# Kernel tuning notes

Measured on AMD Instinct MI355X. Metric: run time of the kernel, lower is better.

The kernel has to match this reference:

```python
import jax, jax.numpy as jnp
import numpy as np

N, E = 3200, 50000
RBF, HID = 16, 128
CUT = 5.0
NS, NV = 32, 16            # multiplicities of 0e and 1o blocks
D = NS + 3 * NV            # 80 = node/message irrep dim
WNUM = NS*NS + NV*NS + NS*NV + NV*NV  # 2304 tensor-product weights per edge
EPS = 1e-8
# path normalization (fully-connected TP, 2 paths per output irrep)
A1 = 1.0 / np.sqrt(2.0 * NS)
A2 = 1.0 / np.sqrt(2.0 * NV)
A3 = 1.0 / np.sqrt(2.0 * NS)
A4 = 1.0 / np.sqrt(2.0 * NV)
ISQ3 = 1.0 / np.sqrt(3.0)


def setup_inputs() -> dict:
    key = jax.random.key(0)
    ks = jax.random.split(key, 24)
    nrm = lambda k, s, sc=1.0: jax.random.normal(k, s, jnp.float32) * sc
    x = nrm(ks[0], (N, D))
    edge_src = jax.random.randint(ks[1], (E,), 0, N)
    edge_dst = jax.random.randint(ks[2], (E,), 0, N)
    dirs = nrm(ks[3], (E, 3))
    unit = dirs / jnp.linalg.norm(dirs, axis=1, keepdims=True)
    # component-normalized SH for l=0,1: [1, sqrt(3)*r_hat]
    edge_sh = jnp.concatenate([jnp.ones((E, 1), jnp.float32), np.sqrt(3.0) * unit], axis=1)
    edge_rbf = nrm(ks[4], (E, RBF))
    edge_len = jax.random.uniform(ks[5], (E,), jnp.float32, 0.1, 6.0)  # some beyond cutoff
    inp = dict(x=x, edge_src=edge_src, edge_dst=edge_dst, edge_sh=edge_sh,
               edge_rbf=edge_rbf, edge_len=edge_len)
    # IrrepNorm affine params
    inp['norm_w'] = jnp.ones((D,), jnp.float32)
    inp['norm_b'] = jnp.zeros((D,), jnp.float32)
    # radial weight MLP (RBF -> HID -> HID -> WNUM)
    inp['mw1'] = nrm(ks[6], (RBF, HID), 1.0/np.sqrt(RBF)); inp['mb1'] = jnp.zeros((HID,), jnp.float32)
    inp['mw2'] = nrm(ks[7], (HID, HID), 1.0/np.sqrt(HID)); inp['mb2'] = jnp.zeros((HID,), jnp.float32)
    inp['mw3'] = nrm(ks[8], (HID, WNUM), 1.0/np.sqrt(HID)); inp['mb3'] = jnp.zeros((WNUM,), jnp.float32)
    # edge gate MLP (RBF -> HID -> 1)
    inp['gw1'] = nrm(ks[9], (RBF, HID), 1.0/np.sqrt(RBF)); inp['gb1'] = jnp.zeros((HID,), jnp.float32)
    inp['gw2'] = nrm(ks[10], (HID, 1), 1.0/np.sqrt(HID)); inp['gb2'] = jnp.zeros((1,), jnp.float32)
    # equivariant linears (e3nn stores N(0,1) weights, normalizes by 1/sqrt(fan_in))
    inp['Ws'] = nrm(ks[11], (NS, NS + NV))   # msg_linear scalar part: 32 -> 32 scalars + 16 gates
    inp['Wv'] = nrm(ks[12], (NV, NV))        # msg_linear vector part
    inp['Us'] = nrm(ks[13], (NS, NS))        # update_linear
    inp['Uv'] = nrm(ks[14], (NV, NV))
    inp['Ss'] = nrm(ks[15], (NS, NS))        # self_linear
    inp['Sv'] = nrm(ks[16], (NV, NV))
    inp['res_scale'] = jnp.float32(0.1)
    return inp


def _irrep_norm(x, w, b):
    s = x[:, :NS]
    v = x[:, NS:].reshape(-1, NV, 3)
    mean = s.mean(axis=1, keepdims=True)
    var = ((s - mean) ** 2).mean(axis=1, keepdims=True)
    s = (s - mean) / jnp.sqrt(var + EPS)
    rms = jnp.sqrt((v ** 2).mean(axis=2, keepdims=True) + EPS)
    v = v / rms
    out = jnp.concatenate([s, v.reshape(-1, 3 * NV)], axis=-1)
    return out * w + b


def reference(x, edge_src, edge_dst, edge_sh, edge_rbf, edge_len,
              norm_w, norm_b, mw1, mb1, mw2, mb2, mw3, mb3,
              gw1, gb1, gw2, gb2, Ws, Wv, Us, Uv, Ss, Sv, res_scale):
    silu = jax.nn.silu
    x_norm = _irrep_norm(x, norm_w, norm_b)                  # [N, 80]
    # radial tensor-product weights per edge
    h = silu(edge_rbf @ mw1 + mb1)
    h = silu(h @ mw2 + mb2)
    tpw = h @ mw3 + mb3                                      # [E, 2304]
    o1 = NS*NS; o2 = o1 + NV*NS; o3 = o2 + NS*NV
    w1 = tpw[:, :o1].reshape(-1, NS, NS)
    w2 = tpw[:, o1:o2].reshape(-1, NV, NS)
    w3 = tpw[:, o2:o3].reshape(-1, NS, NV)
    w4 = tpw[:, o3:].reshape(-1, NV, NV)
    # gather source node features
    xs = x_norm[edge_src, :NS]                               # [E, 32]
    xv = x_norm[edge_src, NS:].reshape(-1, NV, 3)            # [E, 16, 3]
    sh0 = edge_sh[:, 0]                                      # [E]
    sh1 = edge_sh[:, 1:4]                                    # [E, 3]
    # fully-connected TP paths
    msg_s = A1 * jnp.einsum('ei,eio->eo', xs * sh0[:, None], w1)
    inner = jnp.einsum('eim,em->ei', xv, sh1) * ISQ3         # 1o x 1o -> 0e
    msg_s = msg_s + A2 * jnp.einsum('ei,eio->eo', inner, w2)
    msg_v = A3 * jnp.einsum('ei,eio->eo', xs, w3)[:, :, None] * sh1[:, None, :]
    msg_v = msg_v + A4 * jnp.einsum('eim,eio->eom', xv, w4) * sh0[:, None, None]
    m = jnp.concatenate([msg_s, msg_v.reshape(-1, 3 * NV)], axis=-1)  # [E, 80]
    # cutoff envelope and learned edge gate
    cutoff_w = 0.5 * (jnp.cos(jnp.pi * edge_len / CUT) + 1.0) * (edge_len <= CUT).astype(x.dtype)
    gate_w = jax.nn.sigmoid(silu(edge_rbf @ gw1 + gb1) @ gw2 + gb2)   # [E, 1]
    edge_w = cutoff_w[:, None] * gate_w                               # [E, 1]
    m = m * edge_w
    # scatter-add aggregate + normalization
    agg = jax.ops.segment_sum(m, edge_dst, num_segments=N)            # [N, 80]
    den = jax.ops.segment_sum(edge_w, edge_dst, num_segments=N)       # [N, 1]
    agg = agg / jnp.maximum(den, 1e-8)
    # msg_linear -> scalars + gates + gated vectors
    ag_s = agg[:, :NS]
    ag_v = agg[:, NS:].reshape(-1, NV, 3)
    sc = (ag_s @ Ws) / np.sqrt(NS)                                    # [N, 48]
    vc = jnp.einsum('nim,io->nom', ag_v, Wv) / np.sqrt(NV)            # [N, 16, 3]
    s_g = silu(sc[:, :NS])
    gates = jax.nn.sigmoid(sc[:, NS:])
    v_g = vc * gates[:, :, None]
    # update + self interaction
    upd_s = (s_g @ Us) / np.sqrt(NS)
    upd_v = jnp.einsum('nim,io->nom', v_g, Uv) / np.sqrt(NV)
    self_s = (x_norm[:, :NS] @ Ss) / np.sqrt(NS)
    self_v = jnp.einsum('nim,io->nom', x_norm[:, NS:].reshape(-1, NV, 3), Sv) / np.sqrt(NV)
    out = jnp.concatenate([self_s + upd_s, (self_v + upd_v).reshape(-1, 3 * NV)], axis=-1)
    return x + res_scale * out
```

## Files before the change

kernel.cpp:

```cpp
#include <hip/hip_runtime.h>
#include <hip/hip_bf16.h>
#include <math.h>

#define N_NODES 3200
#define E_EDGES 50000
#define RBFN 16
#define HID 128
#define NS 32
#define NV 16
#define DD 80
#define WNUM 2304
#define CUTF 5.0f
#define EPSF 1e-8f

#define A1C 0.125f
#define A2C 0.17677669529663687f
#define A3C 0.125f
#define A4C 0.17677669529663687f
#define A2ISQ 0.10206207261596575f

typedef __attribute__((ext_vector_type(4))) float f32x4;
typedef __attribute__((ext_vector_type(8))) short bf16x8;

__device__ __forceinline__ float sigm(float x) { return 1.0f / (1.0f + __expf(-x)); }
__device__ __forceinline__ float silu_f(float x) { return x * sigm(x); }

__device__ __forceinline__ short bf16r(float x) {
    union { float f; unsigned u; } v; v.f = x;
    unsigned r = (v.u + 0x7fffu + ((v.u >> 16) & 1u)) >> 16;
    return (short)r;
}
__device__ __forceinline__ float b2f(unsigned short s) {
    union { float f; unsigned u; } v; v.u = ((unsigned)s) << 16; return v.f;
}

__global__ void k_scan(const int* __restrict__ hist, int* __restrict__ start) {
    __shared__ int part[256];
    int t = threadIdx.x;
    int loc[13];
    int s = 0;
#pragma unroll
    for (int j = 0; j < 13; j++) {
        int idx = t * 13 + j;
        int v = (idx < N_NODES) ? hist[idx] : 0;
        loc[j] = s; s += v;
    }
    part[t] = s;
    __syncthreads();
    for (int off = 1; off < 256; off <<= 1) {
        int v = part[t];
        int add = (t >= off) ? part[t - off] : 0;
        __syncthreads();
        part[t] = v + add;
        __syncthreads();
    }
    int pre = (t == 0) ? 0 : part[t - 1];
#pragma unroll
    for (int j = 0; j < 13; j++) {
        int idx = t * 13 + j;
        if (idx < N_NODES) start[idx] = pre + loc[j];
    }
    if (t == 255) start[N_NODES] = part[255];
}

__global__ void k_scatter(const int* __restrict__ edst, const int* __restrict__ start,
                          int* __restrict__ cur, int* __restrict__ perm) {
    int e = blockIdx.x * 256 + threadIdx.x;
    if (e < E_EDGES) {
        int d = edst[e];
        int pos = start[d] + atomicAdd(&cur[d], 1);
        perm[pos] = e;
    }
}

__global__ void k_prep0(const float* __restrict__ mw2, __hip_bfloat16* __restrict__ mw2f) {
    __shared__ __hip_bfloat16 st[2048];
    int t = blockIdx.x, tid = threadIdx.x;
    for (int idx = tid; idx < 2048; idx += 256) {
        int k = idx >> 4, c = idx & 15;
        float v = mw2[k * HID + t * 16 + c];
        int kk = k >> 5, q4 = (k >> 3) & 3, j = k & 7;
        st[kk * 512 + (q4 * 16 + c) * 8 + j] = __float2bfloat16(v);
    }
    __syncthreads();
    ((bf16x8*)(mw2f + t * 2048))[tid] = ((const bf16x8*)st)[tid];
}

__global__ __launch_bounds__(256) void k_front(
    const float* __restrict__ rbf, const float* __restrict__ elen,
    const int* __restrict__ edst,
    const float* __restrict__ mw1, const float* __restrict__ mb1,
    const float* __restrict__ gw1, const float* __restrict__ gb1,
    const float* __restrict__ gw2, const float* __restrict__ gb2,
    const float* __restrict__ mb2, const __hip_bfloat16* __restrict__ mw2f,
    const float* __restrict__ mw3, const float* __restrict__ mb3,
    const float* __restrict__ x, const float* __restrict__ nw, const float* __restrict__ nb,
    float* __restrict__ ewg, __hip_bfloat16* __restrict__ h2b,
    __hip_bfloat16* __restrict__ mw3f, __hip_bfloat16* __restrict__ biasf,
    float* __restrict__ xn, int* __restrict__ hist) {
    __shared__ __align__(16) char smem[16640];
    int b = blockIdx.x, tid = threadIdx.x;
    if (b < 782) {
        __hip_bfloat16* h1l = (__hip_bfloat16*)smem;
        int wid = __builtin_amdgcn_readfirstlane(tid >> 6);
        int lane = tid & 63;
        int base = b * 64;
        int eb = base + wid * 16;
        {
            int c0 = lane, c1 = 64 + lane;
            float t0[16], t1[16], g0[16], g1[16];
            float b0 = mb1[c0], b1 = mb1[c1], gb0v = gb1[c0], gb1v = gb1[c1];
#pragma unroll
            for (int e = 0; e < 16; e++) { t0[e] = b0; t1[e] = b1; g0[e] = gb0v; g1[e] = gb1v; }
#pragma unroll
            for (int r = 0; r < RBFN; r++) {
                float w0 = mw1[r * HID + c0], w1 = mw1[r * HID + c1];
                float v0 = gw1[r * HID + c0], v1 = gw1[r * HID + c1];
#pragma unroll
                for (int e = 0; e < 16; e++) {
                    int ee = eb + e; if (ee >= E_EDGES) ee = E_EDGES - 1;
                    float rv = rbf[ee * RBFN + r];
                    t0[e] += rv * w0; t1[e] += rv * w1;
                    g0[e] += rv * v0; g1[e] += rv * v1;
                }
            }
            float q0 = gw2[c0], q1 = gw2[c1];
            float gb2v = gb2[0];
#pragma unroll
            for (int e = 0; e < 16; e++) {
                int le = wid * 16 + e;
                h1l[le * 128 + c0] = __float2bfloat16(silu_f(t0[e]));
                h1l[le * 128 + c1] = __float2bfloat16(silu_f(t1[e]));
                float p = silu_f(g0[e]) * q0 + silu_f(g1[e]) * q1;
                p += __shfl_xor(p, 1);  p += __shfl_xor(p, 2);  p += __shfl_xor(p, 4);
                p += __shfl_xor(p, 8);  p += __shfl_xor(p, 16); p += __shfl_xor(p, 32);
                if (lane == 0 && eb + e < E_EDGES) {
                    float len = elen[eb + e];
                    float cut = (len <= CUTF) ? 0.5f * (cosf(3.14159265358979f * len / CUTF) + 1.0f) : 0.f;
                    ewg[eb + e] = cut * sigm(p + gb2v);
                }
            }
        }
        __syncthreads();
        {
            int q4 = lane >> 4, l15 = lane & 15;
            int le = wid * 16 + l15;
            bf16x8 af[4];
#pragma unroll
            for (int kk = 0; kk < 4; kk++)
                af[kk] = *(const bf16x8*)(h1l + le * 128 + kk * 32 + q4 * 8);
            const f32x4 zf = {0.f, 0.f, 0.f, 0.f};
#pragma unroll
            for (int ct = 0; ct < 8; ct++) {
                f32x4 acc = zf;
#pragma unroll
                for (int kk = 0; kk < 4; kk++) {
                    bf16x8 bw = *(const bf16x8*)(mw2f + (ct * 4 + kk) * 512 + lane * 8);
                    acc = __builtin_amdgcn_mfma_f32_16x16x32_bf16(af[kk], bw, acc, 0, 0, 0);
                }
                float bias = mb2[ct * 16 + l15];
#pragma unroll
                for (int r = 0; r < 4; r++) {
                    int ge = base + wid * 16 + q4 * 4 + r;
                    if (ge < E_EDGES)
                        h2b[ge * HID + ct * 16 + l15] = __float2bfloat16(silu_f(acc[r] + bias));
                }
            }
        }
    } else if (b < 927) {
        int b2 = b - 782;
        __hip_bfloat16* st = (__hip_bfloat16*)smem;
        if (b2 < 144) {
            for (int idx = tid; idx < 2048; idx += 256) {
                int k = idx >> 4, c = idx & 15;
                float v = mw3[k * WNUM + b2 * 16 + c];
                int kk = k >> 5, q4 = (k >> 3) & 3, j = k & 7;
                st[kk * 512 + (q4 * 16 + c) * 8 + j] = __float2bfloat16(v);
            }
            __syncthreads();
            ((bf16x8*)(mw3f + b2 * 2048))[tid] = ((const bf16x8*)st)[tid];
        } else {
            for (int idx = tid; idx < 3072; idx += 256) {
                float val;
                if (idx < 1024) {
                    int oh = idx >> 9, l = (idx >> 3) & 63, j = idx & 7;
                    int o = oh * 16 + (l & 15), i = (l >> 4) * 8 + j;
                    val = mb3[i * 32 + o];
                } else if (idx < 2048) {
                    int t = idx - 1024;
                    int oh = t >> 9, l = (t >> 3) & 63, j = t & 7;
                    int o = oh * 16 + (l & 15), i = (l >> 4) * 8 + j;
                    val = (i < 16) ? mb3[1024 + i * 32 + o] : 0.f;
                } else if (idx < 2560) {
                    int t = idx - 2048;
                    int l = t >> 3, j = t & 7;
                    int o = l & 15, i = (l >> 4) * 8 + j;
                    val = mb3[1536 + i * 16 + o];
                } else {
                    int t = idx - 2560;
                    int l = t >> 3, j = t & 7;
                    int o = l & 15, i = (l >> 4) * 8 + j;
                    val = (i < 16) ? mb3[2048 + i * 16 + o] : 0.f;
                }
                biasf[idx] = __float2bfloat16(val);
            }
        }
    } else if (b < 1727) {
        float* row = (float*)smem;
        int sub = tid >> 6, t = tid & 63;
        int n = (b - 927) * 4 + sub;
        float* rw = row + sub * 80;
        const float* xr = x + n * DD;
        rw[t] = xr[t];
        if (t < 16) rw[64 + t] = xr[64 + t];
        __syncthreads();
        float mean = 0.f;
#pragma unroll
        for (int i = 0; i < NS; i++) mean += rw[i];
        mean *= (1.0f / NS);
        float var = 0.f;
#pragma unroll
        for (int i = 0; i < NS; i++) { float d = rw[i] - mean; var += d * d; }
        var *= (1.0f / NS);
        float inv = rsqrtf(var + EPSF);
        if (t < NS) xn[n * DD + t] = (rw[t] - mean) * inv * nw[t] + nb[t];
        if (t < 48) {
            int j = t / 3;
            float v0 = rw[NS + 3 * j], v1 = rw[NS + 3 * j + 1], v2 = rw[NS + 3 * j + 2];
            float rms = sqrtf((v0 * v0 + v1 * v1 + v2 * v2) * (1.0f / 3.0f) + EPSF);
            xn[n * DD + NS + t] = rw[NS + t] / rms * nw[NS + t] + nb[NS + t];
        }
    } else {
        int e = (b - 1727) * 256 + tid;
        if (e < E_EDGES) atomicAdd(&hist[edst[e]], 1);
    }
}

__global__ __launch_bounds__(256) void k_msg(
    const float* __restrict__ xn, const __hip_bfloat16* __restrict__ h2b,
    const float* __restrict__ ewg, const int* __restrict__ esrc,
    const int* __restrict__ edst, const int* __restrict__ perm,
    const float* __restrict__ esh,
    const __hip_bfloat16* __restrict__ mw3f, const __hip_bfloat16* __restrict__ biasf,
    const int* __restrict__ startp, float* __restrict__ agg, float* __restrict__ agg2,
    float* __restrict__ den) {
    __shared__ __align__(16) char pool[76800];
    unsigned short (*xng)[84]  = (unsigned short(*)[84])(pool);
    unsigned short (*innr)[16] = (unsigned short(*)[16])(pool + 43008);
    float (*sh1l)[4] = (float(*)[4])(pool + 51200);
    float* sh0l = (float*)(pool + 55296);
    float* ewl  = (float*)(pool + 56320);
    int* dstl   = (int*)(pool + 57344);
    int* srcl   = (int*)(pool + 58368);
    int* gel    = (int*)(pool + 59392);
    char* abuf  = pool + 60416;
    float* msgl = (float*)pool;

    const int tid = threadIdx.x;
    const int wid = __builtin_amdgcn_readfirstlane(tid >> 6);
    const int lane = tid & 63;
    const int q4 = lane >> 4;
    const int l15 = lane & 15;
    const int ib = q4 * 8;
    const int grp = blockIdx.x / 3;
    const int slice = blockIdx.x - 3 * grp;
    const int e0 = grp * 256;

    {
        int slot = e0 + tid;
        bool v = slot < E_EDGES;
        int ge = v ? perm[slot] : 0;
        gel[tid] = ge;
        srcl[tid] = esrc[ge];
        dstl[tid] = v ? edst[ge] : -1;
        ewl[tid] = v ? ewg[ge] : 0.f;
        sh0l[tid] = esh[ge * 4];
        sh1l[tid][0] = esh[ge * 4 + 1];
        sh1l[tid][1] = esh[ge * 4 + 2];
        sh1l[tid][2] = esh[ge * 4 + 3];
    }
    __syncthreads();
    {
        int lo = (slice == 0) ? 0 : ((slice == 1) ? 24 : 0);
        int hi = (slice == 0) ? 32 : 80;
        int nv4 = (hi - lo) >> 2;
        for (int idx = tid; idx < 256 * nv4; idx += 256) {
            int e = idx / nv4, k = idx - e * nv4;
            int q = lo + (k << 2);
            f32x4 v = *(const f32x4*)(xn + srcl[e] * 80 + q);
            unsigned p0 = ((unsigned)(unsigned short)bf16r(v[0])) |
                          (((unsigned)(unsigned short)bf16r(v[1])) << 16);
            unsigned p1 = ((unsigned)(unsigned short)bf16r(v[2])) |
                          (((unsigned)(unsigned short)bf16r(v[3])) << 16);
            unsigned* d = (unsigned*)&xng[e][q];
            d[0] = p0; d[1] = p1;
        }
    }
    __syncthreads();
    if (slice == 1) {
        for (int idx = tid; idx < 256 * 16; idx += 256) {
            int e = idx >> 4, i = idx & 15;
            float d = b2f(xng[e][32 + 3 * i]) * sh1l[e][0]
                    + b2f(xng[e][32 + 3 * i + 1]) * sh1l[e][1]
                    + b2f(xng[e][32 + 3 * i + 2]) * sh1l[e][2];
            innr[e][i] = (unsigned short)bf16r(A2ISQ * d);
        }
        __syncthreads();
    }

    int el[4];
#pragma unroll
    for (int et = 0; et < 4; et++) el[et] = wid * 64 + et * 16 + l15;
    bf16x8 hfr[4][4];
#pragma unroll
    for (int et = 0; et < 4; et++) {
        int ge = gel[el[et]];
        const __hip_bfloat16* hr = h2b + ge * HID;
#pragma unroll
        for (int kk = 0; kk < 4; kk++)
            hfr[et][kk] = *(const bf16x8*)(hr + kk * 32 + ib);
    }
    const f32x4 zf = {0.f, 0.f, 0.f, 0.f};
    int cnt = E_EDGES - e0; if (cnt > 256) cnt = 256;

    if (slice < 2) {
        const int nlo = slice * 24, nhi = nlo + 24;
        float f1[4];
        f32x4 msgS[2][4];
#pragma unroll
        for (int et = 0; et < 4; et++) {
            f1[et] = A1C * sh0l[el[et]];
            if (slice == 0) {
                bf16x8 p18;
#pragma unroll
                for (int j = 0; j < 8; j++)
                    p18[j] = bf16r(b2f(xng[el[et]][ib + j]) * f1[et]);
                bf16x8 ba1a = *(const bf16x8*)(biasf + lane * 8);
                bf16x8 ba1b = *(const bf16x8*)(biasf + 512 + lane * 8);
                msgS[0][et] = __builtin_amdgcn_mfma_f32_16x16x32_bf16(ba1a, p18, zf, 0, 0, 0);
                msgS[1][et] = __builtin_amdgcn_mfma_f32_16x16x32_bf16(ba1b, p18, zf, 0, 0, 0);
            } else {
                bf16x8 p28;
#pragma unroll
                for (int j = 0; j < 8; j++)
                    p28[j] = (ib + j < 16) ? (short)innr[el[et]][ib + j] : (short)0;
                bf16x8 ba2a = *(const bf16x8*)(biasf + 1024 + lane * 8);
                bf16x8 ba2b = *(const bf16x8*)(biasf + 1536 + lane * 8);
                msgS[0][et] = __builtin_amdgcn_mfma_f32_16x16x32_bf16(ba2a, p28, zf, 0, 0, 0);
                msgS[1][et] = __builtin_amdgcn_mfma_f32_16x16x32_bf16(ba2b, p28, zf, 0, 0, 0);
            }
        }
        auto computeA = [&](int n, bf16x8 (&A)[8]) {
            f32x4 acc[2][4];
#pragma unroll
            for (int half = 0; half < 2; half++)
#pragma unroll
                for (int et = 0; et < 4; et++) acc[half][et] = zf;
#pragma unroll
            for (int half = 0; half < 2; half++)
#pragma unroll
                for (int kk = 0; kk < 4; kk++)
#pragma unroll
                    for (int et = 0; et < 4; et++)
                        acc[half][et] = __builtin_amdgcn_mfma_f32_16x16x32_bf16(
                            A[half * 4 + kk], hfr[et][kk], acc[half][et], 0, 0, 0);
            float p[4];
            if (n < 32) {
#pragma unroll
                for (int et = 0; et < 4; et++) p[et] = f1[et] * b2f(xng[el[et]][n]);
            } else {
#pragma unroll
                for (int et = 0; et < 4; et++) p[et] = b2f(innr[el[et]][n - 32]);
            }
#pragma unroll
            for (int half = 0; half < 2; half++)
#pragma unroll
                for (int et = 0; et < 4; et++)
#pragma unroll
                    for (int r = 0; r < 4; r++)
                        msgS[half][et][r] += p[et] * acc[half][et][r];
        };
        f32x4 st0, st1;
        {
            const f32x4* src = (const f32x4*)mw3f + nlo * 512 + wid * 128 + lane;
            st0 = src[0]; st1 = src[64];
            f32x4* dst = (f32x4*)abuf + wid * 128 + lane;
            dst[0] = st0; dst[64] = st1;
            __syncthreads();
        }
        for (int n = nlo; n < nhi; ++n) {
            int cb = (n - nlo) & 1;
            if (n + 1 < nhi) {
                const f32x4* src = (const f32x4*)mw3f + (n + 1) * 512 + wid * 128 + lane;
                st0 = src[0]; st1 = src[64];
            }
            bf16x8 A[8];
            const bf16x8* ab = (const bf16x8*)(abuf + cb * 8192);
#pragma unroll
            for (int f = 0; f < 8; f++) A[f] = ab[f * 64 + lane];
            computeA(n, A);
            if (n + 1 < nhi) {
                f32x4* dst = (f32x4*)(abuf + (cb ^ 1) * 8192) + wid * 128 + lane;
                dst[0] = st0; dst[64] = st1;
            }
            __syncthreads();
        }
#pragma unroll
        for (int et = 0; et < 4; et++) {
            int le = el[et];
            float ew = ewl[le];
#pragma unroll
            for (int oh = 0; oh < 2; oh++)
#pragma unroll
                for (int r = 0; r < 4; r++)
                    msgl[le * 48 + oh * 16 + q4 * 4 + r] = msgS[oh][et][r] * ew;
        }
        __syncthreads();
        {
            int nch = (slice == 0) ? 33 : 32;
            int c = lane;
            int r0 = wid * 64;
            int rend = (cnt < r0 + 64) ? cnt : (r0 + 64);
            if (c < nch && r0 < cnt) {
                int cur = dstl[r0];
                float acc = 0.f;
                for (int r = r0; r < rend; r++) {
                    int nd = dstl[r];
                    if (nd != cur) {
                        if (cur >= 0) {
                            bool interior = (startp[cur] >= e0 + r0) && (startp[cur + 1] <= e0 + rend);
                            float* p = (c == 32) ? (den + cur)
                                     : ((slice == 0) ? (agg + cur * 80 + c) : (agg2 + cur * 32 + c));
                            if (interior) *p = acc; else atomicAdd(p, acc);
                        }
                        acc = 0.f; cur = nd;
                    }
                    acc += (c == 32) ? ewl[r] : msgl[r * 48 + c];
                }
                if (cur >= 0) {
                    bool interior = (startp[cur] >= e0 + r0) && (startp[cur + 1] <= e0 + rend);
                    float* p = (c == 32) ? (den + cur)
                             : ((slice == 0) ? (agg + cur * 80 + c) : (agg2 + cur * 32 + c));
                    if (interior) *p = acc; else atomicAdd(p, acc);
                }
            }
        }
    } else {
        const int nlo = 48, nhi = 72;
        float f4e[4];
        f32x4 q3[4], qv[3][4];
#pragma unroll
        for (int et = 0; et < 4; et++) {
            f4e[et] = A4C * sh0l[el[et]];
            bf16x8 xs8;
#pragma unroll
            for (int j = 0; j < 8; j++) xs8[j] = (short)xng[el[et]][ib + j];
            bf16x8 ba3 = *(const bf16x8*)(biasf + 2048 + lane * 8);
            bf16x8 ba4 = *(const bf16x8*)(biasf + 2560 + lane * 8);
            q3[et] = __builtin_amdgcn_mfma_f32_16x16x32_bf16(ba3, xs8, zf, 0, 0, 0);
#pragma unroll
            for (int m = 0; m < 3; m++) {
                bf16x8 t8;
#pragma unroll
                for (int j = 0; j < 8; j++) {
                    int i = ib + j;
                    t8[j] = (i < 16) ? (short)xng[el[et]][32 + 3 * i + m] : (short)0;
                }
                qv[m][et] = __builtin_amdgcn_mfma_f32_16x16x32_bf16(ba4, t8, zf, 0, 0, 0);
            }
        }
        auto computeB = [&](int n, bf16x8 (&A)[8]) {
            f32x4 acc[2][4];
#pragma unroll
            for (int half = 0; half < 2; half++)
#pragma unroll
                for (int et = 0; et < 4; et++) acc[half][et] = zf;
#pragma unroll
            for (int half = 0; half < 2; half++)
#pragma unroll
                for (int kk = 0; kk < 4; kk++)
#pragma unroll
                    for (int et = 0; et < 4; et++)
                        acc[half][et] = __builtin_amdgcn_mfma_f32_16x16x32_bf16(
                            A[half * 4 + kk], hfr[et][kk], acc[half][et], 0, 0, 0);
            if (n < 64) {
#pragma unroll
                for (int half = 0; half < 2; half++) {
                    int i = 2 * (n - 48) + half;
                    float p[4];
#pragma unroll
                    for (int et = 0; et < 4; et++) p[et] = b2f(xng[el[et]][i]);
#pragma unroll
                    for (int et = 0; et < 4; et++)
#pragma unroll
                        for (int r = 0; r < 4; r++)
                            q3[et][r] += p[et] * acc[half][et][r];
                }
            } else {
#pragma unroll
                for (int half = 0; half < 2; half++) {
                    int i = 2 * (n - 64) + half;
#pragma unroll
                    for (int m = 0; m < 3; m++) {
                        float p[4];
#pragma unroll
                        for (int et = 0; et < 4; et++) p[et] = b2f(xng[el[et]][32 + 3 * i + m]);
#pragma unroll
                        for (int et = 0; et < 4; et++)
#pragma unroll
                            for (int r = 0; r < 4; r++)
                                qv[m][et][r] += p[et] * acc[half][et][r];
                    }
                }
            }
        };
        f32x4 st0, st1;
        {
            const f32x4* src = (const f32x4*)mw3f + nlo * 512 + wid * 128 + lane;
            st0 = src[0]; st1 = src[64];
            f32x4* dst = (f32x4*)abuf + wid * 128 + lane;
            dst[0] = st0; dst[64] = st1;
            __syncthreads();
        }
        for (int n = nlo; n < nhi; ++n) {
            int cb = (n - nlo) & 1;
            if (n + 1 < nhi) {
                const f32x4* src = (const f32x4*)mw3f + (n + 1) * 512 + wid * 128 + lane;
                st0 = src[0]; st1 = src[64];
            }
            bf16x8 A[8];
            const bf16x8* ab = (const bf16x8*)(abuf + cb * 8192);
#pragma unroll
            for (int f = 0; f < 8; f++) A[f] = ab[f * 64 + lane];
            computeB(n, A);
            if (n + 1 < nhi) {
                f32x4* dst = (f32x4*)(abuf + (cb ^ 1) * 8192) + wid * 128 + lane;
                dst[0] = st0; dst[64] = st1;
            }
            __syncthreads();
        }
#pragma unroll
        for (int et = 0; et < 4; et++) {
            int le = el[et];
            float ew = ewl[le];
            float s0 = sh1l[le][0], s1 = sh1l[le][1], s2 = sh1l[le][2];
            float b4 = f4e[et];
#pragma unroll
            for (int r = 0; r < 4; r++) {
                int o = q4 * 4 + r;
                float qq = A3C * q3[et][r];
                msgl[le * 48 + o * 3 + 0] = (qq * s0 + b4 * qv[0][et][r]) * ew;
                msgl[le * 48 + o * 3 + 1] = (qq * s1 + b4 * qv[1][et][r]) * ew;
                msgl[le * 48 + o * 3 + 2] = (qq * s2 + b4 * qv[2][et][r]) * ew;
            }
        }
        __syncthreads();
        {
            int c = lane;
            int r0 = wid * 64;
            int rend = (cnt < r0 + 64) ? cnt : (r0 + 64);
            if (c < 48 && r0 < cnt) {
                int cur = dstl[r0];
                float acc = 0.f;
                for (int r = r0; r < rend; r++) {
                    int nd = dstl[r];
                    if (nd != cur) {
                        if (cur >= 0) {
                            bool interior = (startp[cur] >= e0 + r0) && (startp[cur + 1] <= e0 + rend);
                            float* p = agg + cur * 80 + 32 + c;
                            if (interior) *p = acc; else atomicAdd(p, acc);
                        }
                        acc = 0.f; cur = nd;
                    }
                    acc += msgl[r * 48 + c];
                }
                if (cur >= 0) {
                    bool interior = (startp[cur] >= e0 + r0) && (startp[cur + 1] <= e0 + rend);
                    float* p = agg + cur * 80 + 32 + c;
                    if (interior) *p = acc; else atomicAdd(p, acc);
                }
            }
        }
    }
}

__global__ void k_update(
    const float* __restrict__ x, const float* __restrict__ xn,
    const float* __restrict__ agg, const float* __restrict__ agg2,
    const float* __restrict__ den,
    const float* __restrict__ Ws, const float* __restrict__ Wv,
    const float* __restrict__ Us, const float* __restrict__ Uv,
    const float* __restrict__ Ss, const float* __restrict__ Sv,
    const float* __restrict__ rsp, float* __restrict__ out) {
    int n = blockIdx.x, t = threadIdx.x;
    __shared__ float ag[DD];
    __shared__ float xnl[DD];
    __shared__ float sg[NS];
    __shared__ float gt[NV];
    __shared__ float vg[48];
    float idv = 1.0f / fmaxf(den[n], 1e-8f);
    float base = agg[n * DD + t];
    if (t < 32) base += agg2[n * 32 + t];
    ag[t] = base * idv;
    if (t < 16) ag[64 + t] = agg[n * DD + 64 + t] * idv;
    xnl[t] = xn[n * DD + t];
    if (t < 16) xnl[64 + t] = xn[n * DD + 64 + t];
    __syncthreads();
    const float iqs = 0.17677669529663687f;
    const float iqv = 0.25f;
    if (t < 48) {
        float acc = 0.f;
#pragma unroll
        for (int i = 0; i < NS; i++) acc += ag[i] * Ws[i * 48 + t];
        acc *= iqs;
        if (t < NS) sg[t] = silu_f(acc);
        else gt[t - NS] = sigm(acc);
    }
    __syncthreads();
    if (t < 48) {
        int o = t / 3, m = t - 3 * o;
        float acc = 0.f;
#pragma unroll
        for (int i = 0; i < NV; i++) acc += ag[NS + 3 * i + m] * Wv[i * NV + o];
        vg[t] = acc * iqv * gt[o];
    }
    __syncthreads();
    float rs = rsp[0];
    if (t < NS) {
        float us = 0.f, ss = 0.f;
#pragma unroll
        for (int i = 0; i < NS; i++) { us += sg[i] * Us[i * NS + t]; ss += xnl[i] * Ss[i * NS + t]; }
        out[n * DD + t] = x[n * DD + t] + rs * ((ss + us) * iqs);
    }
    if (t < 48) {
        int o = t / 3, m = t - 3 * o;
        float uv = 0.f, sv = 0.f;
#pragma unroll
        for (int i = 0; i < NV; i++) { uv += vg[3 * i + m] * Uv[i * NV + o]; sv += xnl[NS + 3 * i + m] * Sv[i * NV + o]; }
        out[n * DD + NS + t] = x[n * DD + NS + t] + rs * ((sv + uv) * iqv);
    }
}

extern "C" void kernel_launch(void* const* d_in, const int* in_sizes, int n_in,
                              void* d_out, int out_size, void* d_ws, size_t ws_size,
                              hipStream_t stream) {
    (void)in_sizes; (void)n_in; (void)out_size; (void)ws_size;
    const float* x    = (const float*)d_in[0];
    const int*   esrc = (const int*)d_in[1];
    const int*   edst = (const int*)d_in[2];
    const float* esh  = (const float*)d_in[3];
    const float* erbf = (const float*)d_in[4];
    const float* elen = (const float*)d_in[5];
    const float* nw   = (const float*)d_in[6];
    const float* nb   = (const float*)d_in[7];
    const float* mw1  = (const float*)d_in[8];
    const float* mb1  = (const float*)d_in[9];
    const float* mw2  = (const float*)d_in[10];
    const float* mb2  = (const float*)d_in[11];
    const float* mw3  = (const float*)d_in[12];
    const float* mb3  = (const float*)d_in[13];
    const float* gw1  = (const float*)d_in[14];
    const float* gb1  = (const float*)d_in[15];
    const float* gw2  = (const float*)d_in[16];
    const float* gb2  = (const float*)d_in[17];
    const float* Ws   = (const float*)d_in[18];
    const float* Wv   = (const float*)d_in[19];
    const float* Us   = (const float*)d_in[20];
    const float* Uv   = (const float*)d_in[21];
    const float* Ss   = (const float*)d_in[22];
    const float* Sv   = (const float*)d_in[23];
    const float* rsp  = (const float*)d_in[24];
    float* out = (float*)d_out;
    float* ws  = (float*)d_ws;

    float* agg    = ws;
    float* den    = ws + 256000;
    int*   hist   = (int*)(ws + 259200);
    int*   cur    = (int*)(ws + 262400);
    int*   startp = (int*)(ws + 265600);
    int*   perm   = (int*)(ws + 268801);
    float* xn     = ws + 318804;
    float* ewg    = ws + 574804;
    __hip_bfloat16* h2b   = (__hip_bfloat16*)(ws + 624804);
    __hip_bfloat16* mw3f  = (__hip_bfloat16*)(ws + 3824804);
    __hip_bfloat16* biasf = (__hip_bfloat16*)(ws + 3972260);
    __hip_bfloat16* mw2f  = (__hip_bfloat16*)(ws + 3973796);
    float* agg2   = ws + 3981988;

    hipMemsetAsync(ws, 0, 265600 * sizeof(float), stream);
    hipMemsetAsync(agg2, 0, 102400 * sizeof(float), stream);
    k_prep0<<<8, 256, 0, stream>>>(mw2, mw2f);
    k_front<<<1923, 256, 0, stream>>>(erbf, elen, edst, mw1, mb1, gw1, gb1, gw2, gb2,
                                      mb2, mw2f, mw3, mb3, x, nw, nb,
                                      ewg, h2b, mw3f, biasf, xn, hist);
    k_scan<<<1, 256, 0, stream>>>(hist, startp);
    k_scatter<<<196, 256, 0, stream>>>(edst, startp, cur, perm);
    k_msg<<<588, 256, 0, stream>>>(xn, h2b, ewg, esrc, edst, perm, esh,
                                   mw3f, biasf, startp, agg, agg2, den);
    k_update<<<N_NODES, 64, 0, stream>>>(x, xn, agg, agg2, den, Ws, Wv, Us, Uv, Ss, Sv, rsp, out);
}
```

Baseline: 282.0 us.

## Split message kernel into 128-edge blocks with five output slices, drop LDS weight staging

The message kernel now uses 128-thread blocks covering 128 edges, split into five slices instead of three. Four slices each compute half of a scalar output group and the fifth computes the vector paths. The mw3 weight tiles are now read directly from global memory into registers with a two-step software prefetch, replacing the LDS double buffer and its per-iteration barriers. LDS drops from about 75KB to 29KB and launch bounds now target 3 blocks per CU, aiming for higher occupancy and parallelism. The cost is more redundant gathering of edge and h2 features across slices and more global weight loads per block.

```diff
diff --git a/kernel.cpp b/kernel.cpp
--- a/kernel.cpp
+++ b/kernel.cpp
@@ -236,7 +236,7 @@
     }
 }
 
-__global__ __launch_bounds__(256) void k_msg(
+__global__ __launch_bounds__(128, 3) void k_msg(
     const float* __restrict__ xn, const __hip_bfloat16* __restrict__ h2b,
     const float* __restrict__ ewg, const int* __restrict__ esrc,
     const int* __restrict__ edst, const int* __restrict__ perm,
@@ -244,16 +244,15 @@
     const __hip_bfloat16* __restrict__ mw3f, const __hip_bfloat16* __restrict__ biasf,
     const int* __restrict__ startp, float* __restrict__ agg, float* __restrict__ agg2,
     float* __restrict__ den) {
-    __shared__ __align__(16) char pool[76800];
-    unsigned short (*xng)[84]  = (unsigned short(*)[84])(pool);
-    unsigned short (*innr)[16] = (unsigned short(*)[16])(pool + 43008);
-    float (*sh1l)[4] = (float(*)[4])(pool + 51200);
-    float* sh0l = (float*)(pool + 55296);
-    float* ewl  = (float*)(pool + 56320);
-    int* dstl   = (int*)(pool + 57344);
-    int* srcl   = (int*)(pool + 58368);
-    int* gel    = (int*)(pool + 59392);
-    char* abuf  = pool + 60416;
+    __shared__ __align__(16) char pool[29696];
+    unsigned short (*xng)[82]  = (unsigned short(*)[82])(pool);
+    unsigned short (*innr)[16] = (unsigned short(*)[16])(pool + 20992);
+    float* sh0l = (float*)(pool + 25088);
+    int* srcl   = (int*)(pool + 25600);
+    int* gel    = (int*)(pool + 26112);
+    int* dstl   = (int*)(pool + 26624);
+    float* ewl  = (float*)(pool + 27136);
+    float (*sh1l)[4] = (float(*)[4])(pool + 27648);
     float* msgl = (float*)pool;
 
     const int tid = threadIdx.x;
@@ -262,9 +261,9 @@
     const int q4 = lane >> 4;
     const int l15 = lane & 15;
     const int ib = q4 * 8;
-    const int grp = blockIdx.x / 3;
-    const int slice = blockIdx.x - 3 * grp;
-    const int e0 = grp * 256;
+    const int grp = blockIdx.x / 5;
+    const int slice = blockIdx.x - 5 * grp;
+    const int e0 = grp * 128;
 
     {
         int slot = e0 + tid;
@@ -281,10 +280,12 @@
     }
     __syncthreads();
     {
-        int lo = (slice == 0) ? 0 : ((slice == 1) ? 24 : 0);
-        int hi = (slice == 0) ? 32 : 80;
+        int lo, hi;
+        if (slice < 2)      { lo = 0;  hi = 32; }
+        else if (slice < 4) { lo = 24; hi = 80; }
+        else                { lo = 0;  hi = 80; }
         int nv4 = (hi - lo) >> 2;
-        for (int idx = tid; idx < 256 * nv4; idx += 256) {
+        for (int idx = tid; idx < 128 * nv4; idx += 128) {
             int e = idx / nv4, k = idx - e * nv4;
             int q = lo + (k << 2);
             f32x4 v = *(const f32x4*)(xn + srcl[e] * 80 + q);
@@ -297,8 +298,8 @@
         }
     }
     __syncthreads();
-    if (slice == 1) {
-        for (int idx = tid; idx < 256 * 16; idx += 256) {
+    if (slice == 2 || slice == 3) {
+        for (int idx = tid; idx < 128 * 16; idx += 128) {
             int e = idx >> 4, i = idx & 15;
             float d = b2f(xng[e][32 + 3 * i]) * sh1l[e][0]
                     + b2f(xng[e][32 + 3 * i + 1]) * sh1l[e][1]
@@ -321,49 +322,42 @@
             hfr[et][kk] = *(const bf16x8*)(hr + kk * 32 + ib);
     }
     const f32x4 zf = {0.f, 0.f, 0.f, 0.f};
-    int cnt = E_EDGES - e0; if (cnt > 256) cnt = 256;
-
-    if (slice < 2) {
-        const int nlo = slice * 24, nhi = nlo + 24;
+    const bf16x8* gp = (const bf16x8*)mw3f;
+    int cnt = E_EDGES - e0; if (cnt > 128) cnt = 128;
+
+    if (slice < 4) {
+        const int h = slice & 1;
+        const int ch2 = slice >> 1;
+        const int nlo = ch2 * 24, nhi = nlo + 24;
         float f1[4];
-        f32x4 msgS[2][4];
+        f32x4 msgS[4];
+#pragma unroll
+        for (int et = 0; et < 4; et++) f1[et] = A1C * sh0l[el[et]];
 #pragma unroll
         for (int et = 0; et < 4; et++) {
-            f1[et] = A1C * sh0l[el[et]];
-            if (slice == 0) {
-                bf16x8 p18;
+            bf16x8 pb;
+            if (ch2 == 0) {
 #pragma unroll
                 for (int j = 0; j < 8; j++)
-                    p18[j] = bf16r(b2f(xng[el[et]][ib + j]) * f1[et]);
-                bf16x8 ba1a = *(const bf16x8*)(biasf + lane * 8);
-                bf16x8 ba1b = *(const bf16x8*)(biasf + 512 + lane * 8);
-                msgS[0][et] = __builtin_amdgcn_mfma_f32_16x16x32_bf16(ba1a, p18, zf, 0, 0, 0);
-                msgS[1][et] = __builtin_amdgcn_mfma_f32_16x16x32_bf16(ba1b, p18, zf, 0, 0, 0);
+                    pb[j] = bf16r(b2f(xng[el[et]][ib + j]) * f1[et]);
             } else {
-                bf16x8 p28;
 #pragma unroll
                 for (int j = 0; j < 8; j++)
-                    p28[j] = (ib + j < 16) ? (short)innr[el[et]][ib + j] : (short)0;
-                bf16x8 ba2a = *(const bf16x8*)(biasf + 1024 + lane * 8);
-                bf16x8 ba2b = *(const bf16x8*)(biasf + 1536 + lane * 8);
-                msgS[0][et] = __builtin_amdgcn_mfma_f32_16x16x32_bf16(ba2a, p28, zf, 0, 0, 0);
-                msgS[1][et] = __builtin_amdgcn_mfma_f32_16x16x32_bf16(ba2b, p28, zf, 0, 0, 0);
-            }
-        }
-        auto computeA = [&](int n, bf16x8 (&A)[8]) {
-            f32x4 acc[2][4];
-#pragma unroll
-            for (int half = 0; half < 2; half++)
-#pragma unroll
-                for (int et = 0; et < 4; et++) acc[half][et] = zf;
-#pragma unroll
-            for (int half = 0; half < 2; half++)
-#pragma unroll
-                for (int kk = 0; kk < 4; kk++)
-#pragma unroll
-                    for (int et = 0; et < 4; et++)
-                        acc[half][et] = __builtin_amdgcn_mfma_f32_16x16x32_bf16(
-                            A[half * 4 + kk], hfr[et][kk], acc[half][et], 0, 0, 0);
+                    pb[j] = (ib + j < 16) ? (short)innr[el[et]][ib + j] : (short)0;
+            }
+            bf16x8 ba = *(const bf16x8*)(biasf + (ch2 * 1024 + h * 512) + lane * 8);
+            msgS[et] = __builtin_amdgcn_mfma_f32_16x16x32_bf16(ba, pb, zf, 0, 0, 0);
+        }
+        auto computeS = [&](int n, bf16x8 (&A)[4]) {
+            f32x4 acc[4];
+#pragma unroll
+            for (int et = 0; et < 4; et++) acc[et] = zf;
+#pragma unroll
+            for (int kk = 0; kk < 4; kk++)
+#pragma unroll
+                for (int et = 0; et < 4; et++)
+                    acc[et] = __builtin_amdgcn_mfma_f32_16x16x32_bf16(
+                        A[kk], hfr[et][kk], acc[et], 0, 0, 0);
             float p[4];
             if (n < 32) {
 #pragma unroll
@@ -373,51 +367,41 @@
                 for (int et = 0; et < 4; et++) p[et] = b2f(innr[el[et]][n - 32]);
             }
 #pragma unroll
-            for (int half = 0; half < 2; half++)
-#pragma unroll
-                for (int et = 0; et < 4; et++)
-#pragma unroll
-                    for (int r = 0; r < 4; r++)
-                        msgS[half][et][r] += p[et] * acc[half][et][r];
+            for (int et = 0; et < 4; et++)
+#pragma unroll
+                for (int r = 0; r < 4; r++)
+                    msgS[et][r] += p[et] * acc[et][r];
         };
-        f32x4 st0, st1;
+        bf16x8 A0[4], A1[4];
         {
-            const f32x4* src = (const f32x4*)mw3f + nlo * 512 + wid * 128 + lane;
-            st0 = src[0]; st1 = src[64];
-            f32x4* dst = (f32x4*)abuf + wid * 128 + lane;
-            dst[0] = st0; dst[64] = st1;
-            __syncthreads();
-        }
-        for (int n = nlo; n < nhi; ++n) {
-            int cb = (n - nlo) & 1;
-            if (n + 1 < nhi) {
-                const f32x4* src = (const f32x4*)mw3f + (n + 1) * 512 + wid * 128 + lane;
-                st0 = src[0]; st1 = src[64];
-            }
-            bf16x8 A[8];
-            const bf16x8* ab = (const bf16x8*)(abuf + cb * 8192);
-#pragma unroll
-            for (int f = 0; f < 8; f++) A[f] = ab[f * 64 + lane];
-            computeA(n, A);
-            if (n + 1 < nhi) {
-                f32x4* dst = (f32x4*)(abuf + (cb ^ 1) * 8192) + wid * 128 + lane;
-                dst[0] = st0; dst[64] = st1;
-            }
-            __syncthreads();
-        }
+            const bf16x8* g = gp + nlo * 512 + h * 256;
+#pragma unroll
+            for (int f = 0; f < 4; f++) A0[f] = g[f * 64 + lane];
+        }
+        for (int n = nlo; n < nhi; n += 2) {
+            const bf16x8* g1 = gp + (n + 1) * 512 + h * 256;
+#pragma unroll
+            for (int f = 0; f < 4; f++) A1[f] = g1[f * 64 + lane];
+            computeS(n, A0);
+            if (n + 2 < nhi) {
+                const bf16x8* g2 = gp + (n + 2) * 512 + h * 256;
+#pragma unroll
+                for (int f = 0; f < 4; f++) A0[f] = g2[f * 64 + lane];
+            }
+            computeS(n + 1, A1);
+        }
+        __syncthreads();
 #pragma unroll
         for (int et = 0; et < 4; et++) {
             int le = el[et];
             float ew = ewl[le];
 #pragma unroll
-            for (int oh = 0; oh < 2; oh++)
-#pragma unroll
-                for (int r = 0; r < 4; r++)
-                    msgl[le * 48 + oh * 16 + q4 * 4 + r] = msgS[oh][et][r] * ew;
+            for (int r = 0; r < 4; r++)
+                msgl[le * 16 + q4 * 4 + r] = msgS[et][r] * ew;
         }
         __syncthreads();
         {
-            int nch = (slice == 0) ? 33 : 32;
+            int nch = (slice == 0) ? 17 : 16;
             int c = lane;
             int r0 = wid * 64;
             int rend = (cnt < r0 + 64) ? cnt : (r0 + 64);
@@ -429,35 +413,72 @@
                     if (nd != cur) {
                         if (cur >= 0) {
                             bool interior = (startp[cur] >= e0 + r0) && (startp[cur + 1] <= e0 + rend);
-                            float* p = (c == 32) ? (den + cur)
-                                     : ((slice == 0) ? (agg + cur * 80 + c) : (agg2 + cur * 32 + c));
+                            float* p = (c == 16) ? (den + cur)
+                                     : ((slice == 0) ? (agg + cur * 80 + c)
+                                     :  (slice == 1) ? (agg + cur * 80 + 16 + c)
+                                     :  (slice == 2) ? (agg2 + cur * 32 + c)
+                                                     : (agg2 + cur * 32 + 16 + c));
                             if (interior) *p = acc; else atomicAdd(p, acc);
                         }
                         acc = 0.f; cur = nd;
                     }
-                    acc += (c == 32) ? ewl[r] : msgl[r * 48 + c];
+                    acc += (c == 16) ? ewl[r] : msgl[r * 16 + c];
                 }
                 if (cur >= 0) {
                     bool interior = (startp[cur] >= e0 + r0) && (startp[cur + 1] <= e0 + rend);
-                    float* p = (c == 32) ? (den + cur)
-                             : ((slice == 0) ? (agg + cur * 80 + c) : (agg2 + cur * 32 + c));
+                    float* p = (c == 16) ? (den + cur)
+                             : ((slice == 0) ? (agg + cur * 80 + c)
+                             :  (slice == 1) ? (agg + cur * 80 + 16 + c)
+                             :  (slice == 2) ? (agg2 + cur * 32 + c)
+                                             : (agg2 + cur * 32 + 16 + c));
                     if (interior) *p = acc; else atomicAdd(p, acc);
                 }
             }
         }
     } else {
-        const int nlo = 48, nhi = 72;
         float f4e[4];
-        f32x4 q3[4], qv[3][4];
+#pragma unroll
+        for (int et = 0; et < 4; et++) f4e[et] = A4C * sh0l[el[et]];
+        f32x4 q3[4];
 #pragma unroll
         for (int et = 0; et < 4; et++) {
-            f4e[et] = A4C * sh0l[el[et]];
             bf16x8 xs8;
 #pragma unroll
             for (int j = 0; j < 8; j++) xs8[j] = (short)xng[el[et]][ib + j];
             bf16x8 ba3 = *(const bf16x8*)(biasf + 2048 + lane * 8);
+            q3[et] = __builtin_amdgcn_mfma_f32_16x16x32_bf16(ba3, xs8, zf, 0, 0, 0);
+        }
+        for (int n = 48; n < 64; ++n) {
+            bf16x8 A[8];
+            const bf16x8* g = gp + n * 512;
+#pragma unroll
+            for (int f = 0; f < 8; f++) A[f] = g[f * 64 + lane];
+#pragma unroll
+            for (int half = 0; half < 2; half++) {
+                f32x4 acc[4];
+#pragma unroll
+                for (int et = 0; et < 4; et++) acc[et] = zf;
+#pragma unroll
+                for (int kk = 0; kk < 4; kk++)
+#pragma unroll
+                    for (int et = 0; et < 4; et++)
+                        acc[et] = __builtin_amdgcn_mfma_f32_16x16x32_bf16(
+                            A[half * 4 + kk], hfr[et][kk], acc[et], 0, 0, 0);
+                int i = 2 * (n - 48) + half;
+                float p[4];
+#pragma unroll
+                for (int et = 0; et < 4; et++) p[et] = b2f(xng[el[et]][i]);
+#pragma unroll
+                for (int et = 0; et < 4; et++)
+#pragma unroll
+                    for (int r = 0; r < 4; r++)
+                        q3[et][r] += p[et] * acc[et][r];
+            }
+        }
+        f32x4 qv[3][4];
+#pragma unroll
+        for (int et = 0; et < 4; et++) {
             bf16x8 ba4 = *(const bf16x8*)(biasf + 2560 + lane * 8);
-            q3[et] = __builtin_amdgcn_mfma_f32_16x16x32_bf16(ba3, xs8, zf, 0, 0, 0);
 #pragma unroll
             for (int m = 0; m < 3; m++) {
                 bf16x8 t8;
@@ -469,76 +490,37 @@
                 qv[m][et] = __builtin_amdgcn_mfma_f32_16x16x32_bf16(ba4, t8, zf, 0, 0, 0);
             }
         }
-        auto computeB = [&](int n, bf16x8 (&A)[8]) {
-            f32x4 acc[2][4];
-#pragma unroll
-            for (int half = 0; half < 2; half++)
-#pragma unroll
-                for (int et = 0; et < 4; et++) acc[half][et] = zf;
-#pragma unroll
-            for (int half = 0; half < 2; half++)
+        for (int n = 64; n < 72; ++n) {
+            bf16x8 A[8];
+            const bf16x8* g = gp + n * 512;
+#pragma unroll
+            for (int f = 0; f < 8; f++) A[f] = g[f * 64 + lane];
+#pragma unroll
+            for (int half = 0; half < 2; half++) {
+                f32x4 acc[4];
+#pragma unroll
+                for (int et = 0; et < 4; et++) acc[et] = zf;
 #pragma unroll
                 for (int kk = 0; kk < 4; kk++)
 #pragma unroll
                     for (int et = 0; et < 4; et++)
-                        acc[half][et] = __builtin_amdgcn_mfma_f32_16x16x32_bf16(
-                            A[half * 4 + kk], hfr[et][kk], acc[half][et], 0, 0, 0);
-            if (n < 64) {
-#pragma unroll
-                for (int half = 0; half < 2; half++) {
-                    int i = 2 * (n - 48) + half;
+                        acc[et] = __builtin_amdgcn_mfma_f32_16x16x32_bf16(
+                            A[half * 4 + kk], hfr[et][kk], acc[et], 0, 0, 0);
+                int i = 2 * (n - 64) + half;
+#pragma unroll
+                for (int m = 0; m < 3; m++) {
                     float p[4];
 #pragma unroll
-                    for (int et = 0; et < 4; et++) p[et] = b2f(xng[el[et]][i]);
+                    for (int et = 0; et < 4; et++) p[et] = b2f(xng[el[et]][32 + 3 * i + m]);
 #pragma unroll
                     for (int et = 0; et < 4; et++)
 #pragma unroll
                         for (int r = 0; r < 4; r++)
-                            q3[et][r] += p[et] * acc[half][et][r];
-                }
-            } else {
-#pragma unroll
-                for (int half = 0; half < 2; half++) {
-                    int i = 2 * (n - 64) + half;
-#pragma unroll
-                    for (int m = 0; m < 3; m++) {
-                        float p[4];
-#pragma unroll
-                        for (int et = 0; et < 4; et++) p[et] = b2f(xng[el[et]][32 + 3 * i + m]);
-#pragma unroll
-                        for (int et = 0; et < 4; et++)
-#pragma unroll
-                            for (int r = 0; r < 4; r++)
-                                qv[m][et][r] += p[et] * acc[half][et][r];
-                    }
-                }
-            }
-        };
-        f32x4 st0, st1;
-        {
-            const f32x4* src = (const f32x4*)mw3f + nlo * 512 + wid * 128 + lane;
-            st0 = src[0]; st1 = src[64];
-            f32x4* dst = (f32x4*)abuf + wid * 128 + lane;
-            dst[0] = st0; dst[64] = st1;
-            __syncthreads();
-        }
-        for (int n = nlo; n < nhi; ++n) {
-            int cb = (n - nlo) & 1;
-            if (n + 1 < nhi) {
-                const f32x4* src = (const f32x4*)mw3f + (n + 1) * 512 + wid * 128 + lane;
-                st0 = src[0]; st1 = src[64];
-            }
-            bf16x8 A[8];
-            const bf16x8* ab = (const bf16x8*)(abuf + cb * 8192);
-#pragma unroll
-            for (int f = 0; f < 8; f++) A[f] = ab[f * 64 + lane];
-            computeB(n, A);
-            if (n + 1 < nhi) {
-                f32x4* dst = (f32x4*)(abuf + (cb ^ 1) * 8192) + wid * 128 + lane;
-                dst[0] = st0; dst[64] = st1;
-            }
-            __syncthreads();
-        }
+                            qv[m][et][r] += p[et] * acc[et][r];
+                }
+            }
+        }
+        __syncthreads();
 #pragma unroll
         for (int et = 0; et < 4; et++) {
             int le = el[et];
@@ -695,7 +677,7 @@
                                       ewg, h2b, mw3f, biasf, xn, hist);
     k_scan<<<1, 256, 0, stream>>>(hist, startp);
     k_scatter<<<196, 256, 0, stream>>>(edst, startp, cur, perm);
-    k_msg<<<588, 256, 0, stream>>>(xn, h2b, ewg, esrc, edst, perm, esh,
-                                   mw3f, biasf, startp, agg, agg2, den);
+    k_msg<<<1955, 128, 0, stream>>>(xn, h2b, ewg, esrc, edst, perm, esh,
+                                    mw3f, biasf, startp, agg, agg2, den);
     k_update<<<N_NODES, 64, 0, stream>>>(x, xn, agg, agg2, den, Ws, Wv, Us, Uv, Ss, Sv, rsp, out);
 }
```

New measurement: 262.9 us. -6.8%, faster.
